# Performance work log

Hardware: AMD Instinct MI355X
Metric: run time of the kernel (lower is better)

The kernel has to match this reference:

```python
import jax, jax.numpy as jnp
import numpy as np

B, T_TXT, T_IMG, N_LAT = 4, 2048, 8, 64
DIM, DIM_VIS, HEADS, DIM_HEAD = 2048, 1024, 8, 64
INNER = HEADS * DIM_HEAD
LN_EPS = 1e-5


def setup_inputs() -> dict:
    key = jax.random.key(0)
    ks = jax.random.split(key, 8)
    x = jax.random.normal(ks[0], (B, T_TXT, DIM), dtype=jnp.float32)
    media = jax.random.normal(ks[1], (B, T_IMG, N_LAT, DIM_VIS), dtype=jnp.float32)
    # exactly T_IMG media tokens per batch row at random positions
    pos = jax.random.randint(ks[2], (B, T_IMG), 0, T_TXT)
    media_locations = jnp.zeros((B, T_TXT), dtype=bool).at[jnp.arange(B)[:, None], pos].set(True)
    gamma = jnp.ones((DIM,), dtype=jnp.float32)
    beta = jnp.zeros((DIM,), dtype=jnp.float32)
    Wq = jax.random.normal(ks[3], (DIM, INNER), dtype=jnp.float32) * 0.02
    Wkv = jax.random.normal(ks[4], (DIM_VIS, 2 * INNER), dtype=jnp.float32) * 0.02
    Wout = jax.random.normal(ks[5], (INNER, DIM), dtype=jnp.float32) * 0.02
    return {"x": x, "media": media, "media_locations": media_locations,
            "gamma": gamma, "beta": beta, "Wq": Wq, "Wkv": Wkv, "Wout": Wout}


def _split_heads(t, h):
    b, s, _ = t.shape
    return t.reshape(b, s, h, -1).transpose(0, 2, 1, 3)  # b h s d


def reference(x, media, media_locations, gamma, beta, Wq, Wkv, Wout):
    b, t_txt, _ = x.shape
    _, t_img, n, _ = media.shape
    scale = DIM_HEAD ** (-0.5)

    # LayerNorm
    mu = jnp.mean(x, axis=-1, keepdims=True)
    var = jnp.mean(jnp.square(x - mu), axis=-1, keepdims=True)
    xn = (x - mu) * jax.lax.rsqrt(var + LN_EPS) * gamma + beta

    q = _split_heads(xn @ Wq, HEADS) * scale                # b h i d
    media_f = media.reshape(b, t_img * n, -1)               # b (t n) dv
    kv = media_f @ Wkv
    k, v = jnp.split(kv, 2, axis=-1)
    k = _split_heads(k, HEADS)                              # b h j d
    v = _split_heads(v, HEADS)

    sim = jnp.einsum('bhid,bhjd->bhij', q, k)               # b h i (t n)

    text_time = jnp.cumsum(media_locations.astype(jnp.int32), axis=-1)   # b i
    media_time = jnp.repeat(jnp.arange(1, t_img + 1), n)                 # (t n)
    mask = text_time[:, None, :, None] == media_time[None, None, None, :]

    neg = -jnp.finfo(sim.dtype).max
    sim = jnp.where(mask, sim, neg)
    sim = sim - jax.lax.stop_gradient(jnp.max(sim, axis=-1, keepdims=True))
    attn = jax.nn.softmax(sim, axis=-1)
    # zero attention for text tokens that precede any media
    attn = jnp.where((text_time == 0)[:, None, :, None], 0.0, attn)

    out = jnp.einsum('bhij,bhjd->bhid', attn, v)
    out = out.transpose(0, 2, 1, 3).reshape(b, t_txt, INNER)
    return out @ Wout
```

## Files before the change

### kernel.cpp

```cpp
#include <hip/hip_runtime.h>
#include <hip/hip_bf16.h>
#include <stdint.h>

typedef __bf16 bf16_t;
typedef __bf16 bf16x8 __attribute__((ext_vector_type(8)));
typedef float f32x4 __attribute__((ext_vector_type(4)));

#define NB      4
#define T_TXT   2048
#define T_IMG   8
#define N_LAT   64
#define DIM     2048
#define DIM_VIS 1024
#define HEADS   8
#define DHEAD   64
#define INNER   512

__device__ __forceinline__ void gld_lds16(const void* g, void* l) {
    __builtin_amdgcn_global_load_lds((const __attribute__((address_space(1))) void*)g,
                                     (__attribute__((address_space(3))) void*)l,
                                     16, 0, 0);
}

__global__ __launch_bounds__(256) void transpose_cvt_k(const float* __restrict__ in,
                                                       bf16_t* __restrict__ out,
                                                       int R, int C) {
    __shared__ float tile[32][33];
    int c0 = blockIdx.x * 32, r0 = blockIdx.y * 32;
    int x = threadIdx.x, y = threadIdx.y;
#pragma unroll
    for (int d = 0; d < 4; d++)
        tile[y + d * 8][x] = in[(size_t)(r0 + y + d * 8) * C + c0 + x];
    __syncthreads();
#pragma unroll
    for (int d = 0; d < 4; d++)
        out[(size_t)(c0 + y + d * 8) * R + r0 + x] = (bf16_t)tile[x][y + d * 8];
}

__global__ __launch_bounds__(256) void cvt_k(const float* __restrict__ in,
                                             bf16_t* __restrict__ out) {
    int idx = (blockIdx.x * 256 + threadIdx.x) * 8;
    f32x4 a = *(const f32x4*)(in + idx);
    f32x4 b = *(const f32x4*)(in + idx + 4);
    bf16x8 o;
#pragma unroll
    for (int i = 0; i < 4; i++) { o[i] = (bf16_t)a[i]; o[i + 4] = (bf16_t)b[i]; }
    *(bf16x8*)(out + idx) = o;
}

__global__ __launch_bounds__(256) void ln_k(const float* __restrict__ x,
                                            const float* __restrict__ gamma,
                                            const float* __restrict__ beta,
                                            bf16_t* __restrict__ xn) {
    int row = blockIdx.x;
    int t = threadIdx.x;
    const float* xp = x + (size_t)row * DIM + t * 8;
    f32x4 v0 = *(const f32x4*)xp;
    f32x4 v1 = *(const f32x4*)(xp + 4);
    float f[8];
    float s = 0.f, ss = 0.f;
#pragma unroll
    for (int i = 0; i < 4; i++) { f[i] = v0[i]; f[i + 4] = v1[i]; }
#pragma unroll
    for (int i = 0; i < 8; i++) { s += f[i]; ss += f[i] * f[i]; }
#pragma unroll
    for (int off = 32; off > 0; off >>= 1) { s += __shfl_xor(s, off); ss += __shfl_xor(ss, off); }
    __shared__ float sbuf[4], sbuf2[4];
    int wid = t >> 6, lane = t & 63;
    if (lane == 0) { sbuf[wid] = s; sbuf2[wid] = ss; }
    __syncthreads();
    s  = sbuf[0] + sbuf[1] + sbuf[2] + sbuf[3];
    ss = sbuf2[0] + sbuf2[1] + sbuf2[2] + sbuf2[3];
    float mu  = s * (1.0f / DIM);
    float var = ss * (1.0f / DIM) - mu * mu;
    float rs  = rsqrtf(var + 1e-5f);
    f32x4 g0 = *(const f32x4*)(gamma + t * 8);
    f32x4 g1 = *(const f32x4*)(gamma + t * 8 + 4);
    f32x4 b0 = *(const f32x4*)(beta + t * 8);
    f32x4 b1 = *(const f32x4*)(beta + t * 8 + 4);
    bf16x8 o;
#pragma unroll
    for (int i = 0; i < 4; i++) {
        o[i]     = (bf16_t)((f[i]     - mu) * rs * g0[i] + b0[i]);
        o[i + 4] = (bf16_t)((f[i + 4] - mu) * rs * g1[i] + b1[i]);
    }
    *(bf16x8*)(xn + (size_t)row * DIM + t * 8) = o;
}

template <int TAG, typename OT>
__global__ __launch_bounds__(256) void gemm_bt(const bf16_t* __restrict__ A,
                                               const bf16_t* __restrict__ Bt,
                                               OT* __restrict__ C,
                                               int M, int N, int K, int Kper,
                                               float scale) {
    __shared__ __align__(16) bf16_t lA[128 * 32];
    __shared__ __align__(16) bf16_t lB[128 * 32];
    int tid = threadIdx.x;
    int w = tid >> 6, lane = tid & 63;
    int wm = w >> 1, wn = w & 1;
    int bm0 = blockIdx.y * 128, bn0 = blockIdx.x * 128;
    int z = blockIdx.z;
    int kbase = z * Kper;
    int q = lane >> 4, l16 = lane & 15;

    int c0 = w * 64 + lane;
    int r0 = c0 >> 2, cc0 = c0 & 3;
    int c1 = 256 + c0;
    int r1 = c1 >> 2, cc1 = c1 & 3;
    const bf16_t* pA0 = A + (size_t)(bm0 + r0) * K + kbase + cc0 * 8;
    const bf16_t* pA1 = A + (size_t)(bm0 + r1) * K + kbase + cc1 * 8;
    const bf16_t* pB0 = Bt + (size_t)(bn0 + r0) * K + kbase + cc0 * 8;
    const bf16_t* pB1 = Bt + (size_t)(bn0 + r1) * K + kbase + cc1 * 8;
    bf16_t* lA0 = lA + w * 512;
    bf16_t* lA1 = lA + 2048 + w * 512;
    bf16_t* lB0 = lB + w * 512;
    bf16_t* lB1 = lB + 2048 + w * 512;

    f32x4 acc[4][4];
#pragma unroll
    for (int i = 0; i < 4; i++)
#pragma unroll
        for (int j = 0; j < 4; j++)
            acc[i][j] = (f32x4){0.f, 0.f, 0.f, 0.f};

    for (int k0 = 0; k0 < Kper; k0 += 32) {
        __syncthreads();
        gld_lds16(pA0 + k0, lA0);
        gld_lds16(pA1 + k0, lA1);
        gld_lds16(pB0 + k0, lB0);
        gld_lds16(pB1 + k0, lB1);
        __syncthreads();

        bf16x8 af[4], bfr[4];
#pragma unroll
        for (int mt = 0; mt < 4; mt++)
            af[mt] = *(const bf16x8*)(lA + (wm * 64 + mt * 16 + l16) * 32 + q * 8);
#pragma unroll
        for (int nt = 0; nt < 4; nt++)
            bfr[nt] = *(const bf16x8*)(lB + (wn * 64 + nt * 16 + l16) * 32 + q * 8);
#pragma unroll
        for (int mt = 0; mt < 4; mt++)
#pragma unroll
            for (int nt = 0; nt < 4; nt++)
                acc[mt][nt] = __builtin_amdgcn_mfma_f32_16x16x32_bf16(af[mt], bfr[nt], acc[mt][nt], 0, 0, 0);
    }

    OT* Cz = C + (size_t)z * M * N;
#pragma unroll
    for (int mt = 0; mt < 4; mt++)
#pragma unroll
        for (int nt = 0; nt < 4; nt++)
#pragma unroll
            for (int r = 0; r < 4; r++) {
                int row = bm0 + wm * 64 + mt * 16 + q * 4 + r;
                int col = bn0 + wn * 64 + nt * 16 + l16;
                Cz[(size_t)row * N + col] = (OT)(acc[mt][nt][r] * scale);
            }
}

__global__ __launch_bounds__(256) void reduce4_k(const bf16_t* __restrict__ p,
                                                 bf16_t* __restrict__ o,
                                                 size_t n, float scale) {
    size_t i = ((size_t)blockIdx.x * 256 + threadIdx.x) * 8;
    bf16x8 a0 = *(const bf16x8*)(p + i);
    bf16x8 a1 = *(const bf16x8*)(p + n + i);
    bf16x8 a2 = *(const bf16x8*)(p + 2 * n + i);
    bf16x8 a3 = *(const bf16x8*)(p + 3 * n + i);
    bf16x8 r;
#pragma unroll
    for (int u = 0; u < 8; u++)
        r[u] = (bf16_t)(((float)a0[u] + (float)a1[u] + (float)a2[u] + (float)a3[u]) * scale);
    *(bf16x8*)(o + i) = r;
}

__global__ __launch_bounds__(256) void cumsum_bucket_k(const void* __restrict__ locs,
                                                       int* __restrict__ bstart,
                                                       int* __restrict__ bcnt) {
    int b = blockIdx.x, t = threadIdx.x;
    const unsigned* up = (const unsigned*)locs;
    const int* ip = (const int*)locs;
    const unsigned char* bp = (const unsigned char*)locs;
    const float* fp = (const float*)locs;

    int other = 0, nf = 0;
#pragma unroll
    for (int i = 0; i < 8; i++) {
        unsigned wv = up[t * 8 + i];
        nf    += (wv == 0x3F800000u);
        other += (wv != 0u && wv != 1u && wv != 0x3F800000u);
    }
#pragma unroll
    for (int off = 32; off > 0; off >>= 1) { other += __shfl_xor(other, off); nf += __shfl_xor(nf, off); }
    __shared__ int so[4], sf[4];
    int wid = t >> 6, lane = t & 63;
    if (lane == 0) { so[wid] = other; sf[wid] = nf; }
    __syncthreads();
    other = so[0] + so[1] + so[2] + so[3];
    nf    = sf[0] + sf[1] + sf[2] + sf[3];
    int mode = (other > 0) ? 0 : ((nf > 0) ? 2 : 1);

    int v[8];
    int s = 0;
#pragma unroll
    for (int i = 0; i < 8; i++) {
        int idx = b * T_TXT + t * 8 + i;
        int xv;
        if (mode == 1)      xv = ip[idx];
        else if (mode == 0) xv = (int)bp[idx];
        else                xv = (fp[idx] != 0.f) ? 1 : 0;
        v[i] = xv;
        s += xv;
    }
    __shared__ int sc[256];
    __shared__ int sstart[T_IMG];
    if (t < T_IMG) sstart[t] = T_TXT;
    sc[t] = s;
    __syncthreads();
    for (int off = 1; off < 256; off <<= 1) {
        int add = (t >= off) ? sc[t - off] : 0;
        __syncthreads();
        sc[t] += add;
        __syncthreads();
    }
    int run = sc[t] - s;
#pragma unroll
    for (int i = 0; i < 8; i++) {
        run += v[i];
        if (v[i] && run <= T_IMG) sstart[run - 1] = t * 8 + i;
    }
    __syncthreads();
    if (t < T_IMG) {
        int st = sstart[t];
        int nx = (t + 1 < T_IMG) ? sstart[t + 1] : T_TXT;
        bstart[b * T_IMG + t] = st;
        bcnt[b * T_IMG + t]   = nx - st;
    }
}

__global__ __launch_bounds__(256) void attn_mfma_k(const bf16_t* __restrict__ q,
                                                   const bf16_t* __restrict__ kv,
                                                   const int* __restrict__ bstart,
                                                   const int* __restrict__ bcnt,
                                                   bf16_t* __restrict__ aout) {
    __shared__ __align__(16) bf16_t lK[64 * 64];
    __shared__ __align__(16) bf16_t lVt[64 * 64];
    __shared__ __align__(16) bf16_t lP[4][16 * 64];

    int bucket = blockIdx.x >> 3;
    int h = blockIdx.x & 7;
    int n_q = bcnt[bucket];
    if (n_q <= 0) return;
    int b = bucket >> 3;
    int timg = bucket & 7;
    int row0 = b * T_TXT + bstart[bucket];
    size_t krow0 = (size_t)(b * (T_IMG * N_LAT) + timg * N_LAT);

    int tid = threadIdx.x;
    int wid = tid >> 6, lane = tid & 63;
    int quad = lane >> 4, l16 = lane & 15;

    {
        const bf16_t* s0 = kv + (krow0 + 16 * wid + (lane >> 3)) * (2 * INNER) + h * DHEAD + (lane & 7) * 8;
        const bf16_t* s1 = kv + (krow0 + 16 * wid + 8 + (lane >> 3)) * (2 * INNER) + h * DHEAD + (lane & 7) * 8;
        gld_lds16(s0, lK + wid * 1024);
        gld_lds16(s1, lK + wid * 1024 + 512);
    }
    {
        int key = tid & 63, dblk = tid >> 6;
        const bf16_t* vsrc = kv + (krow0 + key) * (2 * INNER) + INNER + h * DHEAD + dblk * 16;
        bf16x8 v0 = *(const bf16x8*)vsrc;
        bf16x8 v1 = *(const bf16x8*)(vsrc + 8);
#pragma unroll
        for (int u = 0; u < 8; u++) {
            lVt[(dblk * 16 + u) * 64 + key]     = v0[u];
            lVt[(dblk * 16 + 8 + u) * 64 + key] = v1[u];
        }
    }
    __syncthreads();

    for (int c0 = wid * 16; c0 < n_q; c0 += 64) {
        int qi = row0 + c0 + ((c0 + l16 < n_q) ? l16 : 0);

        const bf16_t* qrow = q + (size_t)qi * INNER + h * DHEAD + quad * 8;
        bf16x8 qf0 = *(const bf16x8*)qrow;
        bf16x8 qf1 = *(const bf16x8*)(qrow + 32);
        f32x4 s[4];
#pragma unroll
        for (int nt = 0; nt < 4; nt++) s[nt] = (f32x4){0.f, 0.f, 0.f, 0.f};
#pragma unroll
        for (int nt = 0; nt < 4; nt++) {
            bf16x8 kf0 = *(const bf16x8*)(lK + (l16 + 16 * nt) * 64 + quad * 8);
            bf16x8 kf1 = *(const bf16x8*)(lK + (l16 + 16 * nt) * 64 + 32 + quad * 8);
            s[nt] = __builtin_amdgcn_mfma_f32_16x16x32_bf16(qf0, kf0, s[nt], 0, 0, 0);
            s[nt] = __builtin_amdgcn_mfma_f32_16x16x32_bf16(qf1, kf1, s[nt], 0, 0, 0);
        }

        float mr[4];
#pragma unroll
        for (int r = 0; r < 4; r++) {
            float m = fmaxf(fmaxf(s[0][r], s[1][r]), fmaxf(s[2][r], s[3][r]));
#pragma unroll
            for (int off = 8; off >= 1; off >>= 1) m = fmaxf(m, __shfl_xor(m, off));
            mr[r] = m;
        }
        float p[4][4];
#pragma unroll
        for (int nt = 0; nt < 4; nt++)
#pragma unroll
            for (int r = 0; r < 4; r++)
                p[nt][r] = __expf(s[nt][r] - mr[r]);
#pragma unroll
        for (int r = 0; r < 4; r++) {
            float tsum = p[0][r] + p[1][r] + p[2][r] + p[3][r];
#pragma unroll
            for (int off = 8; off >= 1; off >>= 1) tsum += __shfl_xor(tsum, off);
            float inv = 1.0f / tsum;
            p[0][r] *= inv; p[1][r] *= inv; p[2][r] *= inv; p[3][r] *= inv;
        }

        bf16_t* pt = lP[wid];
#pragma unroll
        for (int nt = 0; nt < 4; nt++)
#pragma unroll
            for (int r = 0; r < 4; r++)
                pt[(quad * 4 + r) * 64 + 16 * nt + l16] = (bf16_t)p[nt][r];
        asm volatile("s_waitcnt lgkmcnt(0)" ::: "memory");

        bf16x8 pf0 = *(const bf16x8*)(pt + l16 * 64 + quad * 8);
        bf16x8 pf1 = *(const bf16x8*)(pt + l16 * 64 + 32 + quad * 8);
        f32x4 o[4];
#pragma unroll
        for (int ntd = 0; ntd < 4; ntd++) o[ntd] = (f32x4){0.f, 0.f, 0.f, 0.f};
#pragma unroll
        for (int ntd = 0; ntd < 4; ntd++) {
            bf16x8 vf0 = *(const bf16x8*)(lVt + (l16 + 16 * ntd) * 64 + quad * 8);
            bf16x8 vf1 = *(const bf16x8*)(lVt + (l16 + 16 * ntd) * 64 + 32 + quad * 8);
            o[ntd] = __builtin_amdgcn_mfma_f32_16x16x32_bf16(pf0, vf0, o[ntd], 0, 0, 0);
            o[ntd] = __builtin_amdgcn_mfma_f32_16x16x32_bf16(pf1, vf1, o[ntd], 0, 0, 0);
        }

#pragma unroll
        for (int r = 0; r < 4; r++) {
            int qidx = c0 + quad * 4 + r;
            if (qidx < n_q) {
                bf16_t* op = aout + (size_t)(row0 + qidx) * INNER + h * DHEAD + l16;
#pragma unroll
                for (int ntd = 0; ntd < 4; ntd++)
                    op[16 * ntd] = (bf16_t)o[ntd][r];
            }
        }
    }
}

extern "C" void kernel_launch(void* const* d_in, const int* in_sizes, int n_in,
                              void* d_out, int out_size, void* d_ws, size_t ws_size,
                              hipStream_t stream) {
    const float* x     = (const float*)d_in[0];
    const float* media = (const float*)d_in[1];
    const void*  locs  = d_in[2];
    const float* gamma = (const float*)d_in[3];
    const float* beta  = (const float*)d_in[4];
    const float* Wq    = (const float*)d_in[5];
    const float* Wkv   = (const float*)d_in[6];
    const float* Wout  = (const float*)d_in[7];
    float* out = (float*)d_out;

    bf16_t* xn   = (bf16_t*)d_out;
    bf16_t* part = (bf16_t*)d_out + (size_t)16 * 1024 * 1024;

    char* p = (char*)d_ws;
    bf16_t* qbuf   = (bf16_t*)p; p += (size_t)8192 * 512 * 2;
    bf16_t* aout   = (bf16_t*)p; p += (size_t)8192 * 512 * 2;
    bf16_t* kvbuf  = (bf16_t*)p; p += (size_t)2048 * 1024 * 2;
    bf16_t* mediab = (bf16_t*)p; p += (size_t)2048 * 1024 * 2;
    bf16_t* WqT    = (bf16_t*)p; p += (size_t)512 * 2048 * 2;
    bf16_t* WkvT   = (bf16_t*)p; p += (size_t)1024 * 1024 * 2;
    bf16_t* WoutT  = (bf16_t*)p; p += (size_t)2048 * 512 * 2;
    int*    bstart = (int*)p;    p += 32 * sizeof(int);
    int*    bcnt   = (int*)p;    p += 32 * sizeof(int);

    transpose_cvt_k<<<dim3(512 / 32, 2048 / 32), dim3(32, 8), 0, stream>>>(Wq, WqT, 2048, 512);
    transpose_cvt_k<<<dim3(1024 / 32, 1024 / 32), dim3(32, 8), 0, stream>>>(Wkv, WkvT, 1024, 1024);
    transpose_cvt_k<<<dim3(2048 / 32, 512 / 32), dim3(32, 8), 0, stream>>>(Wout, WoutT, 512, 2048);
    cvt_k<<<(2048 * 1024) / (256 * 8), 256, 0, stream>>>(media, mediab);

    ln_k<<<8192, 256, 0, stream>>>(x, gamma, beta, xn);

    gemm_bt<1, bf16_t><<<dim3(4, 64, 4), 256, 0, stream>>>(xn, WqT, part, 8192, 512, 2048, 512, 1.0f);
    reduce4_k<<<2048, 256, 0, stream>>>(part, qbuf, (size_t)8192 * 512, 0.125f);

    gemm_bt<2, bf16_t><<<dim3(8, 16, 4), 256, 0, stream>>>(mediab, WkvT, part, 2048, 1024, 1024, 256, 1.0f);
    reduce4_k<<<1024, 256, 0, stream>>>(part, kvbuf, (size_t)2048 * 1024, 1.0f);

    cumsum_bucket_k<<<NB, 256, 0, stream>>>(locs, bstart, bcnt);

    hipMemsetAsync(aout, 0, (size_t)8192 * 512 * 2, stream);

    attn_mfma_k<<<32 * HEADS, 256, 0, stream>>>(qbuf, kvbuf, bstart, bcnt, aout);

    gemm_bt<3, float><<<dim3(16, 64, 1), 256, 0, stream>>>(aout, WoutT, out, 8192, 2048, 512, 512, 1.0f);
}
```

Baseline: 270.1 us.

## Double-buffer GEMM LDS, remap workgroups across XCDs, merge weight transposes

The GEMM kernel now keeps two LDS buffers, so the next K-slice loads while the current one is computed, and it uses one barrier per iteration instead of two. Block IDs are flattened to 1D and remapped so that consecutive tiles land on the same XCD (8-way interleave), which should improve L2 reuse on MI355X. The three weight-transpose launches are merged into one kernel to cut launch overhead. LDS use doubles, which may lower occupancy, and the remap assumes the workgroup count divides by 8.

```diff
diff --git a/kernel.cpp b/kernel.cpp
--- a/kernel.cpp
+++ b/kernel.cpp
@@ -22,11 +22,21 @@
                                      16, 0, 0);
 }
 
-__global__ __launch_bounds__(256) void transpose_cvt_k(const float* __restrict__ in,
-                                                       bf16_t* __restrict__ out,
-                                                       int R, int C) {
+__global__ __launch_bounds__(256) void transpose3_k(const float* __restrict__ Wq,
+                                                    const float* __restrict__ Wkv,
+                                                    const float* __restrict__ Wout,
+                                                    bf16_t* __restrict__ WqT,
+                                                    bf16_t* __restrict__ WkvT,
+                                                    bf16_t* __restrict__ WoutT) {
     __shared__ float tile[32][33];
-    int c0 = blockIdx.x * 32, r0 = blockIdx.y * 32;
+    const float* in; bf16_t* out; int R, C;
+    int which = blockIdx.y;
+    if (which == 0)      { in = Wq;   out = WqT;   R = 2048; C = 512;  }
+    else if (which == 1) { in = Wkv;  out = WkvT;  R = 1024; C = 1024; }
+    else                 { in = Wout; out = WoutT; R = 512;  C = 2048; }
+    int nbx = C >> 5;
+    int bx = blockIdx.x % nbx, by = blockIdx.x / nbx;
+    int c0 = bx * 32, r0 = by * 32;
     int x = threadIdx.x, y = threadIdx.y;
 #pragma unroll
     for (int d = 0; d < 4; d++)
@@ -92,15 +102,25 @@
                                                const bf16_t* __restrict__ Bt,
                                                OT* __restrict__ C,
                                                int M, int N, int K, int Kper,
-                                               float scale) {
-    __shared__ __align__(16) bf16_t lA[128 * 32];
-    __shared__ __align__(16) bf16_t lB[128 * 32];
+                                               float scale,
+                                               int gx, int gy, int gz) {
+    __shared__ __align__(16) bf16_t lA[2][128 * 32];
+    __shared__ __align__(16) bf16_t lB[2][128 * 32];
     int tid = threadIdx.x;
     int w = tid >> 6, lane = tid & 63;
     int wm = w >> 1, wn = w & 1;
-    int bm0 = blockIdx.y * 128, bn0 = blockIdx.x * 128;
-    int z = blockIdx.z;
-    int kbase = z * Kper;
+
+    int nwg = gx * gy * gz;
+    int cpx = nwg >> 3;
+    int nid = (blockIdx.x & 7) * cpx + (blockIdx.x >> 3);
+    int tpy = gx * gz;
+    int by = nid / tpy;
+    int rr = nid - by * tpy;
+    int bz = rr / gx;
+    int bx = rr - bz * gx;
+
+    int bm0 = by * 128, bn0 = bx * 128;
+    int kbase = bz * Kper;
     int q = lane >> 4, l16 = lane & 15;
 
     int c0 = w * 64 + lane;
@@ -111,10 +131,6 @@
     const bf16_t* pA1 = A + (size_t)(bm0 + r1) * K + kbase + cc1 * 8;
     const bf16_t* pB0 = Bt + (size_t)(bn0 + r0) * K + kbase + cc0 * 8;
     const bf16_t* pB1 = Bt + (size_t)(bn0 + r1) * K + kbase + cc1 * 8;
-    bf16_t* lA0 = lA + w * 512;
-    bf16_t* lA1 = lA + 2048 + w * 512;
-    bf16_t* lB0 = lB + w * 512;
-    bf16_t* lB1 = lB + 2048 + w * 512;
 
     f32x4 acc[4][4];
 #pragma unroll
@@ -123,29 +139,39 @@
         for (int j = 0; j < 4; j++)
             acc[i][j] = (f32x4){0.f, 0.f, 0.f, 0.f};
 
-    for (int k0 = 0; k0 < Kper; k0 += 32) {
-        __syncthreads();
-        gld_lds16(pA0 + k0, lA0);
-        gld_lds16(pA1 + k0, lA1);
-        gld_lds16(pB0 + k0, lB0);
-        gld_lds16(pB1 + k0, lB1);
-        __syncthreads();
-
+    auto stage = [&](int buf, int k0) {
+        gld_lds16(pA0 + k0, &lA[buf][w * 512]);
+        gld_lds16(pA1 + k0, &lA[buf][2048 + w * 512]);
+        gld_lds16(pB0 + k0, &lB[buf][w * 512]);
+        gld_lds16(pB1 + k0, &lB[buf][2048 + w * 512]);
+    };
+    auto compute = [&](int buf) {
         bf16x8 af[4], bfr[4];
 #pragma unroll
         for (int mt = 0; mt < 4; mt++)
-            af[mt] = *(const bf16x8*)(lA + (wm * 64 + mt * 16 + l16) * 32 + q * 8);
+            af[mt] = *(const bf16x8*)(&lA[buf][(wm * 64 + mt * 16 + l16) * 32 + q * 8]);
 #pragma unroll
         for (int nt = 0; nt < 4; nt++)
-            bfr[nt] = *(const bf16x8*)(lB + (wn * 64 + nt * 16 + l16) * 32 + q * 8);
+            bfr[nt] = *(const bf16x8*)(&lB[buf][(wn * 64 + nt * 16 + l16) * 32 + q * 8]);
 #pragma unroll
         for (int mt = 0; mt < 4; mt++)
 #pragma unroll
             for (int nt = 0; nt < 4; nt++)
                 acc[mt][nt] = __builtin_amdgcn_mfma_f32_16x16x32_bf16(af[mt], bfr[nt], acc[mt][nt], 0, 0, 0);
-    }
-
-    OT* Cz = C + (size_t)z * M * N;
+    };
+
+    stage(0, 0);
+    __syncthreads();
+    int cur = 0;
+    for (int k0 = 32; k0 < Kper; k0 += 32) {
+        stage(cur ^ 1, k0);
+        compute(cur);
+        __syncthreads();
+        cur ^= 1;
+    }
+    compute(cur);
+
+    OT* Cz = C + (size_t)bz * M * N;
 #pragma unroll
     for (int mt = 0; mt < 4; mt++)
 #pragma unroll
@@ -379,17 +405,15 @@
     int*    bstart = (int*)p;    p += 32 * sizeof(int);
     int*    bcnt   = (int*)p;    p += 32 * sizeof(int);
 
-    transpose_cvt_k<<<dim3(512 / 32, 2048 / 32), dim3(32, 8), 0, stream>>>(Wq, WqT, 2048, 512);
-    transpose_cvt_k<<<dim3(1024 / 32, 1024 / 32), dim3(32, 8), 0, stream>>>(Wkv, WkvT, 1024, 1024);
-    transpose_cvt_k<<<dim3(2048 / 32, 512 / 32), dim3(32, 8), 0, stream>>>(Wout, WoutT, 512, 2048);
+    transpose3_k<<<dim3(1024, 3), dim3(32, 8), 0, stream>>>(Wq, Wkv, Wout, WqT, WkvT, WoutT);
     cvt_k<<<(2048 * 1024) / (256 * 8), 256, 0, stream>>>(media, mediab);
 
     ln_k<<<8192, 256, 0, stream>>>(x, gamma, beta, xn);
 
-    gemm_bt<1, bf16_t><<<dim3(4, 64, 4), 256, 0, stream>>>(xn, WqT, part, 8192, 512, 2048, 512, 1.0f);
+    gemm_bt<1, bf16_t><<<1024, 256, 0, stream>>>(xn, WqT, part, 8192, 512, 2048, 512, 1.0f, 4, 64, 4);
     reduce4_k<<<2048, 256, 0, stream>>>(part, qbuf, (size_t)8192 * 512, 0.125f);
 
-    gemm_bt<2, bf16_t><<<dim3(8, 16, 4), 256, 0, stream>>>(mediab, WkvT, part, 2048, 1024, 1024, 256, 1.0f);
+    gemm_bt<2, bf16_t><<<512, 256, 0, stream>>>(mediab, WkvT, part, 2048, 1024, 1024, 256, 1.0f, 8, 16, 4);
     reduce4_k<<<1024, 256, 0, stream>>>(part, kvbuf, (size_t)2048 * 1024, 1.0f);
 
     cumsum_bucket_k<<<NB, 256, 0, stream>>>(locs, bstart, bcnt);
@@ -398,5 +422,5 @@
 
     attn_mfma_k<<<32 * HEADS, 256, 0, stream>>>(qbuf, kvbuf, bstart, bcnt, aout);
 
-    gemm_bt<3, float><<<dim3(16, 64, 1), 256, 0, stream>>>(aout, WoutT, out, 8192, 2048, 512, 512, 1.0f);
-}
+    gemm_bt<3, float><<<1024, 256, 0, stream>>>(aout, WoutT, out, 8192, 2048, 512, 512, 1.0f, 16, 64, 1);
+}
```

New measurement: 260.5 us. 1.04x faster.
